# Performance work log

Measured on AMD Instinct MI355X. Metric: run time of the kernel, lower is better.

Reference implementation:

```python
import jax, jax.numpy as jnp
import numpy as np

B, CIN, COUT, H, W = 8, 128, 256, 64, 64
EPS = 1e-5


def conv2d(x, w, b, pad):
    y = jax.lax.conv_general_dilated(
        x, w, window_strides=(1, 1), padding=[(pad, pad), (pad, pad)],
        dimension_numbers=('NCHW', 'OIHW', 'NCHW'))
    return y + b[None, :, None, None]


def deform_sample(x, offset):
    # x: [B,C,H,W], offset: [B,18,H,W] -> sampled: [B,C,9,H,W]
    b, c, h, w = x.shape
    off = offset.reshape(b, 9, 2, h, w)  # (dy, dx) per kernel tap (torchvision v1 order)
    ky = (jnp.arange(9) // 3 - 1).astype(x.dtype)
    kx = (jnp.arange(9) % 3 - 1).astype(x.dtype)
    py = jnp.arange(h, dtype=x.dtype)[None, None, :, None] + ky[None, :, None, None] + off[:, :, 0]
    px = jnp.arange(w, dtype=x.dtype)[None, None, None, :] + kx[None, :, None, None] + off[:, :, 1]
    y0 = jnp.floor(py); x0 = jnp.floor(px)
    fy = py - y0;       fx = px - x0
    xf = x.reshape(b, c, h * w)

    def gather(iy, ix):
        valid = (iy >= 0) & (iy < h) & (ix >= 0) & (ix < w)
        iyc = jnp.clip(iy, 0, h - 1).astype(jnp.int32)
        ixc = jnp.clip(ix, 0, w - 1).astype(jnp.int32)
        idx = (iyc * w + ixc).reshape(b, -1)  # [B, 9*H*W]
        g = jax.vmap(lambda xb, ib: jnp.take(xb, ib, axis=1))(xf, idx)  # [B,C,9HW]
        return g.reshape(b, c, 9, h, w) * valid.astype(x.dtype)[:, None]

    samp = (gather(y0,     x0    ) * ((1 - fy) * (1 - fx))[:, None]
          + gather(y0,     x0 + 1) * ((1 - fy) * fx      )[:, None]
          + gather(y0 + 1, x0    ) * (fy * (1 - fx)      )[:, None]
          + gather(y0 + 1, x0 + 1) * (fy * fx            )[:, None])
    return samp


def setup_inputs():
    key = jax.random.key(0)
    ks = jax.random.split(key, 8)
    return {
        'x':     jax.random.normal(ks[0], (B, CIN, H, W), jnp.float32),
        'w_off': jax.random.normal(ks[1], (18, CIN, 3, 3), jnp.float32) * 0.01,
        'b_off': jnp.zeros((18,), jnp.float32),
        'w_def': jax.random.normal(ks[2], (COUT, CIN, 3, 3), jnp.float32) * 0.03,
        'b_def': jax.random.normal(ks[3], (COUT,), jnp.float32) * 0.01,
        'gamma': jnp.ones((COUT,), jnp.float32),
        'beta':  jnp.zeros((COUT,), jnp.float32),
        'w_sc':  jax.random.normal(ks[4], (COUT, CIN, 1, 1), jnp.float32) * 0.05,
        'b_sc':  jnp.zeros((COUT,), jnp.float32),
    }


def reference(x, w_off, b_off, w_def, b_def, gamma, beta, w_sc, b_sc):
    offset = conv2d(x, w_off, b_off, pad=1)                 # [B,18,H,W]
    samp = deform_sample(x, offset)                         # [B,C,9,H,W]
    out = jnp.einsum('bckhw,ock->bohw', samp, w_def.reshape(COUT, CIN, 9))
    out = out + b_def[None, :, None, None]
    # BatchNorm2d (training mode: batch statistics)
    mean = out.mean(axis=(0, 2, 3))
    var = out.var(axis=(0, 2, 3))
    out = (out - mean[None, :, None, None]) * jax.lax.rsqrt(var + EPS)[None, :, None, None]
    out = out * gamma[None, :, None, None] + beta[None, :, None, None]
    out = out + conv2d(x, w_sc, b_sc, pad=0)                # residual shortcut (1x1)
    return jax.nn.relu(out)
```

## Files before the change

kernel.cpp:

```cpp
#include <hip/hip_runtime.h>

typedef __attribute__((ext_vector_type(8))) short bf16x8;
typedef __attribute__((ext_vector_type(4))) float f32x4;

__device__ __forceinline__ float bf2f(unsigned short u) {
  return __uint_as_float(((unsigned int)u) << 16);
}
__device__ __forceinline__ unsigned short f2bf(float f) {
  unsigned int u = __float_as_uint(f);
  u += 0x7fffu + ((u >> 16) & 1u);
  return (unsigned short)(u >> 16);
}

constexpr size_t OFF_XPAD = 0;
constexpr size_t SZ_XPAD  = (size_t)8 * 66 * 66 * 128 * 2;
constexpr size_t OFF_WB   = OFF_XPAD + SZ_XPAD;
constexpr size_t SZ_WB    = (size_t)9 * 16 * 256 * 8 * 2;
constexpr size_t OFF_WS2  = OFF_WB + SZ_WB;
constexpr size_t SZ_WS2   = (size_t)16 * 256 * 8 * 2;
constexpr size_t OFF_WO   = OFF_WS2 + SZ_WS2;
constexpr size_t SZ_WO    = (size_t)9 * 16 * 32 * 8 * 2;
constexpr size_t OFF_YM   = OFF_WO + SZ_WO;
constexpr size_t SZ_YM    = (size_t)32768 * 256 * 2;
constexpr size_t OFF_PART = OFF_YM + SZ_YM;
constexpr size_t SZ_PART  = (size_t)512 * 256 * 2 * 4;
constexpr size_t OFF_STAT = OFF_PART + SZ_PART;

__global__ __launch_bounds__(256) void k_prep_x(const float* __restrict__ x,
                                                unsigned short* __restrict__ xp) {
  int blk = blockIdx.x;
  int b = blk >> 6, h = blk & 63;
  int t = threadIdx.x;
  __shared__ float tile[16][66];
  for (int cc = 0; cc < 8; ++cc) {
    int c0 = cc * 16;
    int wr = t & 63, cl = t >> 6;
#pragma unroll
    for (int i = 0; i < 4; ++i) {
      int c = c0 + cl * 4 + i;
      tile[cl * 4 + i][wr] = x[(((size_t)b * 128 + c) * 64 + h) * 64 + wr];
    }
    __syncthreads();
    int ww = t >> 2, cq = t & 3;
    ushort4 u4;
    u4.x = f2bf(tile[cq * 4 + 0][ww]);
    u4.y = f2bf(tile[cq * 4 + 1][ww]);
    u4.z = f2bf(tile[cq * 4 + 2][ww]);
    u4.w = f2bf(tile[cq * 4 + 3][ww]);
    *(ushort4*)(xp + ((size_t)(b * 66 + h + 1) * 66 + (ww + 1)) * 128 + c0 + cq * 4) = u4;
    __syncthreads();
  }
}

__global__ __launch_bounds__(256) void k_pack_w(const float* __restrict__ wdef,
                                                const float* __restrict__ wsc,
                                                const float* __restrict__ woff,
                                                unsigned short* __restrict__ wB,
                                                unsigned short* __restrict__ wS,
                                                unsigned short* __restrict__ wO) {
  int tid = blockIdx.x * 256 + threadIdx.x;
  if (tid < 294912) {
    int k8 = tid & 7, n = (tid >> 3) & 255, kb = (tid >> 11) & 15, tap = tid >> 15;
    int c = kb * 8 + k8;
    wB[tid] = f2bf(wdef[((size_t)n * 128 + c) * 9 + tap]);
  } else if (tid < 294912 + 32768) {
    int i = tid - 294912;
    int k8 = i & 7, n = (i >> 3) & 255, kb = i >> 11;
    wS[i] = f2bf(wsc[(size_t)n * 128 + kb * 8 + k8]);
  } else if (tid < 294912 + 32768 + 36864) {
    int i = tid - 327680;
    int k8 = i & 7, n = (i >> 3) & 31, kb = (i >> 8) & 15, tap = i >> 12;
    int c = kb * 8 + k8;
    wO[i] = f2bf(n < 18 ? woff[((size_t)n * 128 + c) * 9 + tap] : 0.f);
  }
}

__global__ __launch_bounds__(256) void k_main(const unsigned short* __restrict__ xp,
                                              const unsigned short* __restrict__ wB,
                                              const unsigned short* __restrict__ wO,
                                              const float* __restrict__ boff,
                                              const float* __restrict__ bdef,
                                              unsigned short* __restrict__ ymain,
                                              float* __restrict__ partials) {
  int blk = blockIdx.x;
  int b = blk >> 6, h = blk & 63;
  int t = threadIdx.x;
  int lane = t & 63, wid = t >> 6;
  int m = lane & 15, quad = lane >> 4;
  __shared__ __align__(16) unsigned short At[2][64 * 136];
  __shared__ float offsL[9][64][2];

  {
    f32x4 a0 = {0.f, 0.f, 0.f, 0.f}, a1 = {0.f, 0.f, 0.f, 0.f};
    int px = wid * 16 + m;
    const unsigned short* xbase = xp + ((size_t)(b * 66 + h) * 66 + px) * 128 + quad * 8;
    for (int tap = 0; tap < 9; ++tap) {
      const unsigned short* arow = xbase + ((tap / 3) * 66 + (tap % 3)) * 128;
#pragma unroll
      for (int kk = 0; kk < 4; ++kk) {
        bf16x8 a = *(const bf16x8*)(arow + kk * 32);
        const unsigned short* bb = wO + (size_t)(tap * 16 + kk * 4 + quad) * 256;
        bf16x8 b0 = *(const bf16x8*)(bb + m * 8);
        bf16x8 b1 = *(const bf16x8*)(bb + (16 + m) * 8);
        a0 = __builtin_amdgcn_mfma_f32_16x16x32_bf16(a, b0, a0, 0, 0, 0);
        a1 = __builtin_amdgcn_mfma_f32_16x16x32_bf16(a, b1, a1, 0, 0, 0);
      }
    }
#pragma unroll
    for (int r = 0; r < 4; ++r) {
      int pxs = wid * 16 + quad * 4 + r;
      offsL[m >> 1][pxs][m & 1] = a0[r] + boff[m];
      if (m < 2) offsL[8][pxs][m] = a1[r] + boff[16 + m];
    }
  }
  __syncthreads();

  f32x4 acc[4][4];
#pragma unroll
  for (int i = 0; i < 4; ++i)
#pragma unroll
    for (int j = 0; j < 4; ++j) acc[i][j] = (f32x4){0.f, 0.f, 0.f, 0.f};

  int px_s = t >> 2, sub = t & 3;
  const unsigned short* xb_base = xp + (size_t)b * 66 * 66 * 128;
  int nb = wid * 64;

  auto sample_prep = [&](int tap, float* wgt, const unsigned short** p) {
    float2 ov = *(const float2*)&offsL[tap][px_s][0];
    int ky = tap / 3 - 1, kx = tap % 3 - 1;
    float py = (float)(h + ky) + ov.x;
    float pxf = (float)(px_s + kx) + ov.y;
    float y0f = floorf(py), x0f = floorf(pxf);
    float fy = py - y0f, fx = pxf - x0f;
    int iy0 = (int)y0f, ix0 = (int)x0f;
#pragma unroll
    for (int j = 0; j < 4; ++j) {
      int iy = iy0 + (j >> 1), ix = ix0 + (j & 1);
      float wy = (j >> 1) ? fy : 1.f - fy;
      float wx = (j & 1) ? fx : 1.f - fx;
      bool valid = (iy >= 0) && (iy < 64) && (ix >= 0) && (ix < 64);
      int iyc = min(max(iy, 0), 63), ixc = min(max(ix, 0), 63);
      wgt[j] = valid ? wy * wx : 0.f;
      p[j] = xb_base + ((size_t)(iyc + 1) * 66 + (ixc + 1)) * 128 + sub * 8;
    }
  };
  auto load_g2 = [&](const unsigned short** p, int g0, bf16x8 (*v)[4]) {
#pragma unroll
    for (int gg = 0; gg < 2; ++gg)
#pragma unroll
      for (int j = 0; j < 4; ++j)
        v[gg][j] = *(const bf16x8*)(p[j] + (g0 + gg) * 32);
  };
  auto store_g2 = [&](unsigned short* dst, int g0, const float* wgt, bf16x8 (*v)[4]) {
#pragma unroll
    for (int gg = 0; gg < 2; ++gg) {
      bf16x8 o;
#pragma unroll
      for (int j = 0; j < 8; ++j) {
        float s = fmaf(wgt[0], bf2f((unsigned short)v[gg][0][j]),
                  fmaf(wgt[1], bf2f((unsigned short)v[gg][1][j]),
                  fmaf(wgt[2], bf2f((unsigned short)v[gg][2][j]),
                       wgt[3] * bf2f((unsigned short)v[gg][3][j]))));
        o[j] = (short)f2bf(s);
      }
      *(bf16x8*)(dst + (g0 + gg) * 32) = o;
    }
  };
  auto mfma_half = [&](const unsigned short* buf, int tap, int kk0) {
#pragma unroll
    for (int kk = kk0; kk < kk0 + 2; ++kk) {
      bf16x8 af[4];
#pragma unroll
      for (int ms = 0; ms < 4; ++ms)
        af[ms] = *(const bf16x8*)(buf + (ms * 16 + m) * 136 + kk * 32 + quad * 8);
#pragma unroll
      for (int ns = 0; ns < 4; ++ns) {
        bf16x8 bfr = *(const bf16x8*)(wB + ((size_t)(tap * 16 + kk * 4 + quad) * 256 + nb + ns * 16 + m) * 8);
#pragma unroll
        for (int ms = 0; ms < 4; ++ms)
          acc[ms][ns] = __builtin_amdgcn_mfma_f32_16x16x32_bf16(af[ms], bfr, acc[ms][ns], 0, 0, 0);
      }
    }
  };

  {
    float wgt[4]; const unsigned short* p[4]; bf16x8 v[2][4];
    sample_prep(0, wgt, p);
    unsigned short* dst = &At[0][px_s * 136 + sub * 8];
    load_g2(p, 0, v); store_g2(dst, 0, wgt, v);
    load_g2(p, 2, v); store_g2(dst, 2, wgt, v);
  }
#pragma unroll
  for (int tap = 0; tap < 9; ++tap) {
    __syncthreads();
    const unsigned short* cur = At[tap & 1];
    unsigned short* dst = &At[(tap + 1) & 1][px_s * 136 + sub * 8];
    if (tap < 8) {
      float wgt[4]; const unsigned short* p[4]; bf16x8 v[2][4];
      sample_prep(tap + 1, wgt, p);
      load_g2(p, 0, v);
      mfma_half(cur, tap, 0);
      store_g2(dst, 0, wgt, v);
      load_g2(p, 2, v);
      mfma_half(cur, tap, 2);
      store_g2(dst, 2, wgt, v);
    } else {
      mfma_half(cur, tap, 0);
      mfma_half(cur, tap, 2);
    }
  }

  __syncthreads();
  unsigned short* yb = &At[0][0];
#pragma unroll
  for (int ns = 0; ns < 4; ++ns) {
    int n = nb + ns * 16 + m;
    float bias = bdef[n];
    float s = 0.f, q = 0.f;
#pragma unroll
    for (int ms = 0; ms < 4; ++ms) {
#pragma unroll
      for (int r = 0; r < 4; ++r) {
        int px = ms * 16 + quad * 4 + r;
        float v = acc[ms][ns][r] + bias;
        yb[px * 264 + n] = f2bf(v);
        s += v;
        q += v * v;
      }
    }
    s += __shfl_xor(s, 16); s += __shfl_xor(s, 32);
    q += __shfl_xor(q, 16); q += __shfl_xor(q, 32);
    if (quad == 0) {
      partials[((size_t)blk * 256 + n) * 2 + 0] = s;
      partials[((size_t)blk * 256 + n) * 2 + 1] = q;
    }
  }
  __syncthreads();
  {
    unsigned short* grow = ymain + (size_t)(blk * 64 + px_s) * 256;
    const unsigned short* lrow = yb + px_s * 264;
#pragma unroll
    for (int k = 0; k < 8; ++k) {
      int n0 = k * 32 + sub * 8;
      *(bf16x8*)(grow + n0) = *(const bf16x8*)(lrow + n0);
    }
  }
}

__global__ __launch_bounds__(64) void k_stats(const float* __restrict__ partials,
                                              const float* __restrict__ gamma,
                                              const float* __restrict__ beta,
                                              float* __restrict__ stats) {
  int ch = blockIdx.x;
  int L = threadIdx.x;
  float s = 0.f, q = 0.f;
#pragma unroll
  for (int i = 0; i < 8; ++i) {
    int row = i * 64 + L;
    s += partials[((size_t)row * 256 + ch) * 2 + 0];
    q += partials[((size_t)row * 256 + ch) * 2 + 1];
  }
#pragma unroll
  for (int d = 1; d < 64; d <<= 1) { s += __shfl_xor(s, d); q += __shfl_xor(q, d); }
  if (L == 0) {
    float mean = s * (1.f / 32768.f);
    float var = q * (1.f / 32768.f) - mean * mean;
    float inv = rsqrtf(var + 1e-5f);
    float A = gamma[ch] * inv;
    stats[ch * 2 + 0] = A;
    stats[ch * 2 + 1] = beta[ch] - mean * A;
  }
}

__global__ __launch_bounds__(256) void k_final(const unsigned short* __restrict__ xp,
                                               const unsigned short* __restrict__ wS,
                                               const unsigned short* __restrict__ ymain,
                                               const float* __restrict__ stats,
                                               const float* __restrict__ bsc,
                                               float* __restrict__ out) {
  int blk = blockIdx.x;
  int b = blk >> 6, h = blk & 63;
  int t = threadIdx.x;
  int lane = t & 63, wid = t >> 6;
  int m = lane & 15, quad = lane >> 4;
  __shared__ float tr[128 * 67];
  f32x4 acc[4][4];
#pragma unroll
  for (int i = 0; i < 4; ++i)
#pragma unroll
    for (int j = 0; j < 4; ++j) acc[i][j] = (f32x4){0.f, 0.f, 0.f, 0.f};
  const unsigned short* xrow = xp + ((size_t)(b * 66 + h + 1) * 66 + 1) * 128;
  int nb = wid * 64;
#pragma unroll
  for (int kk = 0; kk < 4; ++kk) {
    bf16x8 af[4];
#pragma unroll
    for (int ms = 0; ms < 4; ++ms)
      af[ms] = *(const bf16x8*)(xrow + (ms * 16 + m) * 128 + kk * 32 + quad * 8);
#pragma unroll
    for (int ns = 0; ns < 4; ++ns) {
      bf16x8 bfr = *(const bf16x8*)(wS + ((size_t)(kk * 4 + quad) * 256 + nb + ns * 16 + m) * 8);
#pragma unroll
      for (int ms = 0; ms < 4; ++ms)
        acc[ms][ns] = __builtin_amdgcn_mfma_f32_16x16x32_bf16(af[ms], bfr, acc[ms][ns], 0, 0, 0);
    }
  }
  for (int pass = 0; pass < 2; ++pass) {
    if ((wid >> 1) == pass) {
#pragma unroll
      for (int ns = 0; ns < 4; ++ns) {
        int n = nb + ns * 16 + m;
        float bs = bsc[n];
        int nl = n - pass * 128;
#pragma unroll
        for (int ms = 0; ms < 4; ++ms)
#pragma unroll
          for (int r = 0; r < 4; ++r) {
            int px = ms * 16 + quad * 4 + r;
            tr[nl * 67 + px] = acc[ms][ns][r] + bs;
          }
      }
    }
    __syncthreads();
    {
      int nl = t & 127, g = t >> 7;
      int n = pass * 128 + nl;
      float A = stats[n * 2], Bc = stats[n * 2 + 1];
#pragma unroll 8
      for (int i = 0; i < 32; ++i) {
        int px = g * 32 + i;
        float ym = bf2f(ymain[(size_t)(blk * 64 + px) * 256 + n]);
        float* pt = &tr[nl * 67 + px];
        *pt = fmaxf(fmaf(ym, A, Bc) + *pt, 0.f);
      }
    }
    __syncthreads();
    {
      int ww = t & 63, ng = t >> 6;
#pragma unroll 8
      for (int i = 0; i < 32; ++i) {
        int nl = ng * 32 + i;
        out[((size_t)(b * 256 + pass * 128 + nl) * 64 + h) * 64 + ww] = tr[nl * 67 + ww];
      }
    }
    __syncthreads();
  }
}

extern "C" void kernel_launch(void* const* d_in, const int* in_sizes, int n_in,
                              void* d_out, int out_size, void* d_ws, size_t ws_size,
                              hipStream_t stream) {
  const float* x     = (const float*)d_in[0];
  const float* w_off = (const float*)d_in[1];
  const float* b_off = (const float*)d_in[2];
  const float* w_def = (const float*)d_in[3];
  const float* b_def = (const float*)d_in[4];
  const float* gamma = (const float*)d_in[5];
  const float* beta  = (const float*)d_in[6];
  const float* w_sc  = (const float*)d_in[7];
  const float* b_sc  = (const float*)d_in[8];
  float* out = (float*)d_out;

  char* ws = (char*)d_ws;
  unsigned short* xpad  = (unsigned short*)(ws + OFF_XPAD);
  unsigned short* wB    = (unsigned short*)(ws + OFF_WB);
  unsigned short* wS    = (unsigned short*)(ws + OFF_WS2);
  unsigned short* wO    = (unsigned short*)(ws + OFF_WO);
  unsigned short* ymain = (unsigned short*)(ws + OFF_YM);
  float* partials       = (float*)(ws + OFF_PART);
  float* stats          = (float*)(ws + OFF_STAT);

  hipMemsetAsync(xpad, 0, SZ_XPAD, stream);
  k_prep_x<<<512, 256, 0, stream>>>(x, xpad);
  k_pack_w<<<1424, 256, 0, stream>>>(w_def, w_sc, w_off, wB, wS, wO);
  k_main<<<512, 256, 0, stream>>>(xpad, wB, wO, b_off, b_def, ymain, partials);
  k_stats<<<256, 64, 0, stream>>>(partials, gamma, beta, stats);
  k_final<<<512, 256, 0, stream>>>(xpad, wS, ymain, stats, b_sc, out);
}
```

Measured before the change: 162.1 us.

## Split rows into half-row blocks and zero only padding borders in prep

The main deformable-conv kernel and the final fused kernel now give each block half an image row (32 pixels), so each launches 1024 blocks instead of 512, with smaller LDS tiles and fewer accumulators per thread. The full memset of the padded input is replaced by writing zeros only to the border pixels inside k_prep_x. The stats reduction reads twice as many partials, loaded as float2, and the final kernel reads ymain two channels at a time. More blocks give the GPU more to schedule and less LDS per block, but each block reuses its weight loads across fewer pixels, and the offset conv runs on only half the waves.

```diff
diff --git a/kernel.cpp b/kernel.cpp
--- a/kernel.cpp
+++ b/kernel.cpp
@@ -23,7 +23,7 @@
 constexpr size_t OFF_YM   = OFF_WO + SZ_WO;
 constexpr size_t SZ_YM    = (size_t)32768 * 256 * 2;
 constexpr size_t OFF_PART = OFF_YM + SZ_YM;
-constexpr size_t SZ_PART  = (size_t)512 * 256 * 2 * 4;
+constexpr size_t SZ_PART  = (size_t)1024 * 256 * 2 * 4;
 constexpr size_t OFF_STAT = OFF_PART + SZ_PART;
 
 __global__ __launch_bounds__(256) void k_prep_x(const float* __restrict__ x,
@@ -32,6 +32,23 @@
   int b = blk >> 6, h = blk & 63;
   int t = threadIdx.x;
   __shared__ float tile[16][66];
+
+  {
+    unsigned short* base = xp + (size_t)b * 66 * 66 * 128;
+    ushort4 z4 = {0, 0, 0, 0};
+    if (t < 64) {
+      int col = (t >> 5) ? 65 : 0;
+      int i = t & 31;
+      *(ushort4*)(base + ((size_t)(h + 1) * 66 + col) * 128 + i * 4) = z4;
+    }
+    if (h == 0) {
+      for (int i = t; i < 2112; i += 256) {
+        *(ushort4*)(base + (size_t)i * 4) = z4;
+        *(ushort4*)(base + (size_t)65 * 66 * 128 + (size_t)i * 4) = z4;
+      }
+    }
+  }
+
   for (int cc = 0; cc < 8; ++cc) {
     int c0 = cc * 16;
     int wr = t & 63, cl = t >> 6;
@@ -83,16 +100,17 @@
                                               unsigned short* __restrict__ ymain,
                                               float* __restrict__ partials) {
   int blk = blockIdx.x;
-  int b = blk >> 6, h = blk & 63;
+  int b = blk >> 7, rem = blk & 127, h = rem >> 1, half = rem & 1;
+  int px0 = half * 32;
   int t = threadIdx.x;
   int lane = t & 63, wid = t >> 6;
   int m = lane & 15, quad = lane >> 4;
-  __shared__ __align__(16) unsigned short At[2][64 * 136];
-  __shared__ float offsL[9][64][2];
-
-  {
+  __shared__ __align__(16) unsigned short At[2][32 * 136];
+  __shared__ float offsL[9][32][2];
+
+  if (wid < 2) {
     f32x4 a0 = {0.f, 0.f, 0.f, 0.f}, a1 = {0.f, 0.f, 0.f, 0.f};
-    int px = wid * 16 + m;
+    int px = px0 + wid * 16 + m;
     const unsigned short* xbase = xp + ((size_t)(b * 66 + h) * 66 + px) * 128 + quad * 8;
     for (int tap = 0; tap < 9; ++tap) {
       const unsigned short* arow = xbase + ((tap / 3) * 66 + (tap % 3)) * 128;
@@ -115,13 +133,13 @@
   }
   __syncthreads();
 
-  f32x4 acc[4][4];
-#pragma unroll
-  for (int i = 0; i < 4; ++i)
+  f32x4 acc[2][4];
+#pragma unroll
+  for (int i = 0; i < 2; ++i)
 #pragma unroll
     for (int j = 0; j < 4; ++j) acc[i][j] = (f32x4){0.f, 0.f, 0.f, 0.f};
 
-  int px_s = t >> 2, sub = t & 3;
+  int px_s = t >> 3, sub = t & 7;
   const unsigned short* xb_base = xp + (size_t)b * 66 * 66 * 128;
   int nb = wid * 64;
 
@@ -129,7 +147,7 @@
     float2 ov = *(const float2*)&offsL[tap][px_s][0];
     int ky = tap / 3 - 1, kx = tap % 3 - 1;
     float py = (float)(h + ky) + ov.x;
-    float pxf = (float)(px_s + kx) + ov.y;
+    float pxf = (float)(px0 + px_s + kx) + ov.y;
     float y0f = floorf(py), x0f = floorf(pxf);
     float fy = py - y0f, fx = pxf - x0f;
     int iy0 = (int)y0f, ix0 = (int)x0f;
@@ -144,51 +162,46 @@
       p[j] = xb_base + ((size_t)(iyc + 1) * 66 + (ixc + 1)) * 128 + sub * 8;
     }
   };
-  auto load_g2 = [&](const unsigned short** p, int g0, bf16x8 (*v)[4]) {
-#pragma unroll
-    for (int gg = 0; gg < 2; ++gg)
-#pragma unroll
-      for (int j = 0; j < 4; ++j)
-        v[gg][j] = *(const bf16x8*)(p[j] + (g0 + gg) * 32);
+  auto load_g1 = [&](const unsigned short** p, int g, bf16x8* v) {
+#pragma unroll
+    for (int j = 0; j < 4; ++j)
+      v[j] = *(const bf16x8*)(p[j] + g * 64);
   };
-  auto store_g2 = [&](unsigned short* dst, int g0, const float* wgt, bf16x8 (*v)[4]) {
-#pragma unroll
-    for (int gg = 0; gg < 2; ++gg) {
-      bf16x8 o;
-#pragma unroll
-      for (int j = 0; j < 8; ++j) {
-        float s = fmaf(wgt[0], bf2f((unsigned short)v[gg][0][j]),
-                  fmaf(wgt[1], bf2f((unsigned short)v[gg][1][j]),
-                  fmaf(wgt[2], bf2f((unsigned short)v[gg][2][j]),
-                       wgt[3] * bf2f((unsigned short)v[gg][3][j]))));
-        o[j] = (short)f2bf(s);
-      }
-      *(bf16x8*)(dst + (g0 + gg) * 32) = o;
-    }
+  auto store_g1 = [&](unsigned short* dst, int g, const float* wgt, bf16x8* v) {
+    bf16x8 o;
+#pragma unroll
+    for (int j = 0; j < 8; ++j) {
+      float s = fmaf(wgt[0], bf2f((unsigned short)v[0][j]),
+                fmaf(wgt[1], bf2f((unsigned short)v[1][j]),
+                fmaf(wgt[2], bf2f((unsigned short)v[2][j]),
+                     wgt[3] * bf2f((unsigned short)v[3][j]))));
+      o[j] = (short)f2bf(s);
+    }
+    *(bf16x8*)(dst + g * 64) = o;
   };
   auto mfma_half = [&](const unsigned short* buf, int tap, int kk0) {
 #pragma unroll
     for (int kk = kk0; kk < kk0 + 2; ++kk) {
-      bf16x8 af[4];
-#pragma unroll
-      for (int ms = 0; ms < 4; ++ms)
+      bf16x8 af[2];
+#pragma unroll
+      for (int ms = 0; ms < 2; ++ms)
         af[ms] = *(const bf16x8*)(buf + (ms * 16 + m) * 136 + kk * 32 + quad * 8);
 #pragma unroll
       for (int ns = 0; ns < 4; ++ns) {
         bf16x8 bfr = *(const bf16x8*)(wB + ((size_t)(tap * 16 + kk * 4 + quad) * 256 + nb + ns * 16 + m) * 8);
 #pragma unroll
-        for (int ms = 0; ms < 4; ++ms)
+        for (int ms = 0; ms < 2; ++ms)
           acc[ms][ns] = __builtin_amdgcn_mfma_f32_16x16x32_bf16(af[ms], bfr, acc[ms][ns], 0, 0, 0);
       }
     }
   };
 
   {
-    float wgt[4]; const unsigned short* p[4]; bf16x8 v[2][4];
+    float wgt[4]; const unsigned short* p[4]; bf16x8 v0[4], v1[4];
     sample_prep(0, wgt, p);
     unsigned short* dst = &At[0][px_s * 136 + sub * 8];
-    load_g2(p, 0, v); store_g2(dst, 0, wgt, v);
-    load_g2(p, 2, v); store_g2(dst, 2, wgt, v);
+    load_g1(p, 0, v0); load_g1(p, 1, v1);
+    store_g1(dst, 0, wgt, v0); store_g1(dst, 1, wgt, v1);
   }
 #pragma unroll
   for (int tap = 0; tap < 9; ++tap) {
@@ -196,14 +209,14 @@
     const unsigned short* cur = At[tap & 1];
     unsigned short* dst = &At[(tap + 1) & 1][px_s * 136 + sub * 8];
     if (tap < 8) {
-      float wgt[4]; const unsigned short* p[4]; bf16x8 v[2][4];
+      float wgt[4]; const unsigned short* p[4]; bf16x8 v0[4], v1[4];
       sample_prep(tap + 1, wgt, p);
-      load_g2(p, 0, v);
+      load_g1(p, 0, v0);
+      load_g1(p, 1, v1);
       mfma_half(cur, tap, 0);
-      store_g2(dst, 0, wgt, v);
-      load_g2(p, 2, v);
+      store_g1(dst, 0, wgt, v0);
       mfma_half(cur, tap, 2);
-      store_g2(dst, 2, wgt, v);
+      store_g1(dst, 1, wgt, v1);
     } else {
       mfma_half(cur, tap, 0);
       mfma_half(cur, tap, 2);
@@ -218,7 +231,7 @@
     float bias = bdef[n];
     float s = 0.f, q = 0.f;
 #pragma unroll
-    for (int ms = 0; ms < 4; ++ms) {
+    for (int ms = 0; ms < 2; ++ms) {
 #pragma unroll
       for (int r = 0; r < 4; ++r) {
         int px = ms * 16 + quad * 4 + r;
@@ -237,11 +250,11 @@
   }
   __syncthreads();
   {
-    unsigned short* grow = ymain + (size_t)(blk * 64 + px_s) * 256;
+    unsigned short* grow = ymain + (size_t)(blk * 32 + px_s) * 256;
     const unsigned short* lrow = yb + px_s * 264;
 #pragma unroll
-    for (int k = 0; k < 8; ++k) {
-      int n0 = k * 32 + sub * 8;
+    for (int k = 0; k < 4; ++k) {
+      int n0 = k * 64 + sub * 8;
       *(bf16x8*)(grow + n0) = *(const bf16x8*)(lrow + n0);
     }
   }
@@ -255,10 +268,11 @@
   int L = threadIdx.x;
   float s = 0.f, q = 0.f;
 #pragma unroll
-  for (int i = 0; i < 8; ++i) {
+  for (int i = 0; i < 16; ++i) {
     int row = i * 64 + L;
-    s += partials[((size_t)row * 256 + ch) * 2 + 0];
-    q += partials[((size_t)row * 256 + ch) * 2 + 1];
+    float2 pq = *(const float2*)&partials[((size_t)row * 256 + ch) * 2];
+    s += pq.x;
+    q += pq.y;
   }
 #pragma unroll
   for (int d = 1; d < 64; d <<= 1) { s += __shfl_xor(s, d); q += __shfl_xor(q, d); }
@@ -279,29 +293,30 @@
                                                const float* __restrict__ bsc,
                                                float* __restrict__ out) {
   int blk = blockIdx.x;
-  int b = blk >> 6, h = blk & 63;
+  int b = blk >> 7, rem = blk & 127, h = rem >> 1, half = rem & 1;
+  int px0 = half * 32;
   int t = threadIdx.x;
   int lane = t & 63, wid = t >> 6;
   int m = lane & 15, quad = lane >> 4;
-  __shared__ float tr[128 * 67];
-  f32x4 acc[4][4];
-#pragma unroll
-  for (int i = 0; i < 4; ++i)
+  __shared__ float tr[128 * 35];
+  f32x4 acc[2][4];
+#pragma unroll
+  for (int i = 0; i < 2; ++i)
 #pragma unroll
     for (int j = 0; j < 4; ++j) acc[i][j] = (f32x4){0.f, 0.f, 0.f, 0.f};
-  const unsigned short* xrow = xp + ((size_t)(b * 66 + h + 1) * 66 + 1) * 128;
+  const unsigned short* xrow = xp + ((size_t)(b * 66 + h + 1) * 66 + 1 + px0) * 128;
   int nb = wid * 64;
 #pragma unroll
   for (int kk = 0; kk < 4; ++kk) {
-    bf16x8 af[4];
-#pragma unroll
-    for (int ms = 0; ms < 4; ++ms)
+    bf16x8 af[2];
+#pragma unroll
+    for (int ms = 0; ms < 2; ++ms)
       af[ms] = *(const bf16x8*)(xrow + (ms * 16 + m) * 128 + kk * 32 + quad * 8);
 #pragma unroll
     for (int ns = 0; ns < 4; ++ns) {
       bf16x8 bfr = *(const bf16x8*)(wS + ((size_t)(kk * 4 + quad) * 256 + nb + ns * 16 + m) * 8);
 #pragma unroll
-      for (int ms = 0; ms < 4; ++ms)
+      for (int ms = 0; ms < 2; ++ms)
         acc[ms][ns] = __builtin_amdgcn_mfma_f32_16x16x32_bf16(af[ms], bfr, acc[ms][ns], 0, 0, 0);
     }
   }
@@ -313,34 +328,40 @@
         float bs = bsc[n];
         int nl = n - pass * 128;
 #pragma unroll
-        for (int ms = 0; ms < 4; ++ms)
+        for (int ms = 0; ms < 2; ++ms)
 #pragma unroll
           for (int r = 0; r < 4; ++r) {
             int px = ms * 16 + quad * 4 + r;
-            tr[nl * 67 + px] = acc[ms][ns][r] + bs;
+            tr[nl * 35 + px] = acc[ms][ns][r] + bs;
           }
       }
     }
     __syncthreads();
     {
-      int nl = t & 127, g = t >> 7;
-      int n = pass * 128 + nl;
-      float A = stats[n * 2], Bc = stats[n * 2 + 1];
-#pragma unroll 8
-      for (int i = 0; i < 32; ++i) {
-        int px = g * 32 + i;
-        float ym = bf2f(ymain[(size_t)(blk * 64 + px) * 256 + n]);
-        float* pt = &tr[nl * 67 + px];
-        *pt = fmaxf(fmaf(ym, A, Bc) + *pt, 0.f);
+      int nl2 = t & 63, g = t >> 6;
+      int n = pass * 128 + nl2 * 2;
+      float A0 = stats[n * 2 + 0], B0 = stats[n * 2 + 1];
+      float A1 = stats[n * 2 + 2], B1 = stats[n * 2 + 3];
+#pragma unroll
+      for (int i = 0; i < 8; ++i) {
+        int pxl = g * 8 + i;
+        unsigned int ym2 = *(const unsigned int*)(ymain + (size_t)(blk * 32 + pxl) * 256 + n);
+        float y0 = bf2f((unsigned short)(ym2 & 0xffffu));
+        float y1 = bf2f((unsigned short)(ym2 >> 16));
+        int nl = nl2 * 2;
+        float* p0 = &tr[nl * 35 + pxl];
+        float* p1 = &tr[(nl + 1) * 35 + pxl];
+        *p0 = fmaxf(fmaf(y0, A0, B0) + *p0, 0.f);
+        *p1 = fmaxf(fmaf(y1, A1, B1) + *p1, 0.f);
       }
     }
     __syncthreads();
     {
-      int ww = t & 63, ng = t >> 6;
-#pragma unroll 8
-      for (int i = 0; i < 32; ++i) {
-        int nl = ng * 32 + i;
-        out[((size_t)(b * 256 + pass * 128 + nl) * 64 + h) * 64 + ww] = tr[nl * 67 + ww];
+      int ww = t & 31, ng = t >> 5;
+#pragma unroll
+      for (int i = 0; i < 16; ++i) {
+        int nl = ng * 16 + i;
+        out[((size_t)(b * 256 + pass * 128 + nl) * 64 + h) * 64 + px0 + ww] = tr[nl * 35 + ww];
       }
     }
     __syncthreads();
@@ -370,10 +391,9 @@
   float* partials       = (float*)(ws + OFF_PART);
   float* stats          = (float*)(ws + OFF_STAT);
 
-  hipMemsetAsync(xpad, 0, SZ_XPAD, stream);
   k_prep_x<<<512, 256, 0, stream>>>(x, xpad);
   k_pack_w<<<1424, 256, 0, stream>>>(w_def, w_sc, w_off, wB, wS, wO);
-  k_main<<<512, 256, 0, stream>>>(xpad, wB, wO, b_off, b_def, ymain, partials);
+  k_main<<<1024, 256, 0, stream>>>(xpad, wB, wO, b_off, b_def, ymain, partials);
   k_stats<<<256, 64, 0, stream>>>(partials, gamma, beta, stats);
-  k_final<<<512, 256, 0, stream>>>(xpad, wS, ymain, stats, b_sc, out);
-}
+  k_final<<<1024, 256, 0, stream>>>(xpad, wS, ymain, stats, b_sc, out);
+}
```

Measured after the change: 169.7 us. +4.7%, slower.
